# Optimization experiments

Measured on AMD Instinct MI355X. Metric: run time of the kernel, lower is better.

## Reference

```python
import jax, jax.numpy as jnp
import numpy as np

B, L, E, H, DV, V = 256, 512, 200, 256, 30000, 50000
NEG_INF = -jnp.inf

def setup_inputs() -> dict:
    key = jax.random.key(0)
    ks = jax.random.split(key, 16)
    s = 0.05
    f = jnp.float32
    return {
        "input_id": jax.random.randint(ks[0], (B, 1), 0, V),
        "input_emb": jax.random.normal(ks[1], (B, 1, E), f),
        "encoder_outputs": jax.random.normal(ks[2], (B, L, H), f),
        "encoder_input_ids": jax.random.randint(ks[3], (B, L), 0, V),
        "hidden": jax.random.normal(ks[4], (B, 1, H), f),
        "attention": jax.random.normal(ks[5], (B, 1, H), f),
        # GRU (PyTorch layout): W_ih (3H, 2H+E), W_hh (3H, H), gate order r,z,n
        "W_ih": jax.random.normal(ks[6], (3 * H, 2 * H + E), f) * s,
        "W_hh": jax.random.normal(ks[7], (3 * H, H), f) * s,
        "b_ih": jnp.zeros((3 * H,), f),
        "b_hh": jnp.zeros((3 * H,), f),
        "W_attn": jax.random.normal(ks[8], (H, H), f) * s,
        "b_attn": jnp.zeros((H,), f),
        "W_comb": jax.random.normal(ks[9], (H, 2 * H), f) * s,
        "b_comb": jnp.zeros((H,), f),
        "W_gen": jax.random.normal(ks[10], (DV, H), f) * s,
        "b_gen": jnp.zeros((DV,), f),
        "W_copy": jax.random.normal(ks[11], (H, H), f) * s,
        "b_copy": jnp.zeros((H,), f),
    }


def reference(input_id, input_emb, encoder_outputs, encoder_input_ids, hidden,
              attention, W_ih, W_hh, b_ih, b_hh, W_attn, b_attn, W_comb,
              b_comb, W_gen, b_gen, W_copy, b_copy):
    b, l = encoder_input_ids.shape
    # selective read: rou = normalized match mask (NaN guard -> 0)
    mask = (input_id == encoder_input_ids).astype(encoder_outputs.dtype)  # (b,l)
    msum = jnp.sum(mask, axis=1, keepdims=True)
    rou = jnp.where(msum > 0, mask / jnp.where(msum > 0, msum, 1.0), 0.0)
    selective_read = jnp.einsum('bl,blh->bh', rou, encoder_outputs)  # (b,h)

    # GRU single step (dropout is identity at inference)
    x = jnp.concatenate([input_emb[:, 0], attention[:, 0], selective_read], axis=-1)
    h_prev = hidden[:, 0]  # (b,h)
    gx = x @ W_ih.T + b_ih          # (b,3h)
    gh = h_prev @ W_hh.T + b_hh     # (b,3h)
    xr, xz, xn = jnp.split(gx, 3, axis=-1)
    hr, hz, hn = jnp.split(gh, 3, axis=-1)
    r = jax.nn.sigmoid(xr + hr)
    z = jax.nn.sigmoid(xz + hz)
    n = jnp.tanh(xn + r * hn)
    h = (1.0 - z) * n + z * h_prev  # (b,h) cur_hidden

    # attention
    q = h @ W_attn.T + b_attn
    attn_w = jax.nn.softmax(jnp.einsum('bh,blh->bl', q, encoder_outputs), axis=-1)
    attn_applied = jnp.einsum('bl,blh->bh', attn_w, encoder_outputs)
    cur_attention = jnp.tanh(
        jnp.concatenate([attn_applied, h], axis=-1) @ W_comb.T + b_comb)  # (b,h)

    # generate + copy scores, joint softmax
    generate_score = cur_attention @ W_gen.T + b_gen                     # (b,DV)
    copy_weights = jax.nn.sigmoid(encoder_outputs @ W_copy.T + b_copy)   # (b,l,h)
    copy_score = jnp.einsum('blh,bh->bl', copy_weights, cur_attention)   # (b,l)
    score = jax.nn.softmax(jnp.concatenate([generate_score, copy_score], axis=1), axis=1)
    gen_s, copy_s = score[:, :DV], score[:, DV:]

    # fused equivalent of the one-hot scatter/mix: direct scatter-add into vocab
    output = jnp.zeros((b, V), score.dtype)
    output = output.at[:, :DV].add(gen_s)
    output = output.at[jnp.arange(b)[:, None], encoder_input_ids].add(copy_s)

    pos = output > 0
    out = jnp.where(pos, jnp.log(jnp.where(pos, output, 1.0)), NEG_INF)
    return out, h[:, None, :], cur_attention[:, None, :]
```

## Files before the change

kernel.cpp:

```cpp
#include <hip/hip_runtime.h>
#include <cmath>

#define B_  256
#define L_  512
#define E_  200
#define H_  256
#define DV_ 30000
#define V_  50000
#define X_  712
#define G3_ 768

#define NEG_BIG -1.0e30f

typedef __attribute__((ext_vector_type(8))) _Float16 half8;
typedef __attribute__((ext_vector_type(4))) float   floatx4;

#define GLOAD16(gptr, lptr)                                                            \
    __builtin_amdgcn_global_load_lds(                                                  \
        (const __attribute__((address_space(1))) unsigned int*)(gptr),                 \
        (__attribute__((address_space(3))) unsigned int*)(lptr), 16, 0, 0)

__global__ void k_cast_wc(const float* __restrict__ Wc, _Float16* __restrict__ wcb) {
    int i = blockIdx.x * 256 + threadIdx.x;
    wcb[i] = (_Float16)Wc[i];
}

__global__ void k_selread(const int* __restrict__ input_id, const float* __restrict__ emb,
                          const float* __restrict__ attention, const float* __restrict__ hidden,
                          const float* __restrict__ enc, const int* __restrict__ enc_ids,
                          float* __restrict__ xT) {
    int b = blockIdx.x, t = threadIdx.x;
    __shared__ int cnt;
    __shared__ int list[L_];
    if (t == 0) cnt = 0;
    __syncthreads();
    int id = input_id[b];
    for (int l = t; l < L_; l += 256) {
        if (enc_ids[b * L_ + l] == id) { int p = atomicAdd(&cnt, 1); list[p] = l; }
    }
    __syncthreads();
    int n = cnt;
    float s = 0.f;
    for (int i = 0; i < n; i++) s += enc[(b * L_ + list[i]) * H_ + t];
    float sel = (n > 0) ? s / (float)n : 0.f;
    for (int k = t; k < E_; k += 256) xT[k * B_ + b] = emb[b * E_ + k];
    xT[(E_ + t) * B_ + b]       = attention[b * H_ + t];
    xT[(E_ + H_ + t) * B_ + b]  = sel;
    xT[(X_ + t) * B_ + b]       = hidden[b * H_ + t];
}

template<int K>
__global__ void __launch_bounds__(256) k_gru_one(const float* __restrict__ xTp, const float* __restrict__ W,
                                                 const float* __restrict__ bias, float* __restrict__ g) {
    __shared__ __align__(16) float Ws[8 * K];
    int t  = threadIdx.x;
    int j0 = blockIdx.x * 8;
    int bq = t & 63;
    int jh = t >> 6;
#pragma unroll
    for (int jj = 0; jj < 8; jj++) {
        const float4* src = (const float4*)(W + (size_t)(j0 + jj) * K);
        float4* dst = (float4*)(Ws + jj * K);
        for (int i = t; i < K / 4; i += 256) dst[i] = src[i];
    }
    __syncthreads();
    float acc0[4] = {0.f, 0.f, 0.f, 0.f};
    float acc1[4] = {0.f, 0.f, 0.f, 0.f};
    const float* w0 = Ws + (jh * 2 + 0) * K;
    const float* w1 = Ws + (jh * 2 + 1) * K;
#pragma unroll 2
    for (int k4 = 0; k4 < K / 4; k4++) {
        float4 wa = *(const float4*)(w0 + k4 * 4);
        float4 wb = *(const float4*)(w1 + k4 * 4);
        float wav[4] = {wa.x, wa.y, wa.z, wa.w};
        float wbv[4] = {wb.x, wb.y, wb.z, wb.w};
#pragma unroll
        for (int u = 0; u < 4; u++) {
            float4 xv = *(const float4*)(xTp + (size_t)(k4 * 4 + u) * B_ + bq * 4);
            acc0[0] += wav[u] * xv.x; acc0[1] += wav[u] * xv.y;
            acc0[2] += wav[u] * xv.z; acc0[3] += wav[u] * xv.w;
            acc1[0] += wbv[u] * xv.x; acc1[1] += wbv[u] * xv.y;
            acc1[2] += wbv[u] * xv.z; acc1[3] += wbv[u] * xv.w;
        }
    }
    int ja = j0 + jh * 2, jb = ja + 1;
    float ba = bias[ja], bb = bias[jb];
#pragma unroll
    for (int i = 0; i < 4; i++) {
        g[(size_t)(bq * 4 + i) * G3_ + ja] = acc0[i] + ba;
        g[(size_t)(bq * 4 + i) * G3_ + jb] = acc1[i] + bb;
    }
}

__global__ void k_gru_gates(const float* __restrict__ gx, const float* __restrict__ gh,
                            const float* __restrict__ hidden, float* __restrict__ hws,
                            float* __restrict__ hout) {
    int b = blockIdx.x, j = threadIdx.x;
    float xr = gx[b * G3_ + j], xz = gx[b * G3_ + 256 + j], xn = gx[b * G3_ + 512 + j];
    float hr = gh[b * G3_ + j], hz = gh[b * G3_ + 256 + j], hn = gh[b * G3_ + 512 + j];
    float r = 1.f / (1.f + expf(-(xr + hr)));
    float z = 1.f / (1.f + expf(-(xz + hz)));
    float n = tanhf(xn + r * hn);
    float hp = hidden[b * H_ + j];
    float h = (1.f - z) * n + z * hp;
    hws[b * H_ + j] = h;
    hout[b * H_ + j] = h;
}

__global__ void __launch_bounds__(1024) k_attn(const float* __restrict__ hws, const float* __restrict__ enc,
                       const float* __restrict__ W_attn, const float* __restrict__ b_attn,
                       const float* __restrict__ W_comb, const float* __restrict__ b_comb,
                       float* __restrict__ caws, _Float16* __restrict__ cab,
                       float* __restrict__ caout) {
    int b = blockIdx.x, t = threadIdx.x;
    int lane = t & 63, w = t >> 6;
    int jj = t & 255, ph = t >> 8;
    __shared__ float hs[H_], qs[H_], sc[L_], ap[H_];
    __shared__ float part[4][H_];
    __shared__ float red[20];
    if (t < 256) hs[t] = hws[b * H_ + t];
    __syncthreads();
    {
        const float4* wr = (const float4*)(W_attn + (size_t)jj * H_ + ph * 64);
        const float4* hp = (const float4*)(hs + ph * 64);
        float acc = 0.f;
#pragma unroll
        for (int k4 = 0; k4 < 16; k4++) {
            float4 wv = wr[k4]; float4 hv = hp[k4];
            acc += wv.x * hv.x + wv.y * hv.y + wv.z * hv.z + wv.w * hv.w;
        }
        part[ph][jj] = acc;
    }
    __syncthreads();
    if (t < 256) qs[t] = b_attn[t] + part[0][t] + part[1][t] + part[2][t] + part[3][t];
    __syncthreads();
    {
        float4 q4 = *(const float4*)&qs[lane * 4];
        size_t base = (size_t)b * L_ + w * 32;
        for (int i = 0; i < 32; i += 4) {
            float s[4];
#pragma unroll
            for (int u = 0; u < 4; u++) {
                float4 e = *(const float4*)(enc + (base + i + u) * H_ + lane * 4);
                s[u] = q4.x * e.x + q4.y * e.y + q4.z * e.z + q4.w * e.w;
            }
#pragma unroll
            for (int u = 0; u < 4; u++) {
#pragma unroll
                for (int o = 1; o < 64; o <<= 1) s[u] += __shfl_xor(s[u], o);
                if (lane == 0) sc[w * 32 + i + u] = s[u];
            }
        }
    }
    __syncthreads();
    float ev = 0.f;
    if (t < 512) {
        float m = sc[t];
#pragma unroll
        for (int o = 1; o < 64; o <<= 1) m = fmaxf(m, __shfl_xor(m, o));
        if (lane == 0) red[w] = m;
    }
    __syncthreads();
    if (t == 0) {
        float m = red[0];
        for (int i = 1; i < 8; i++) m = fmaxf(m, red[i]);
        red[16] = m;
    }
    __syncthreads();
    if (t < 512) {
        ev = __expf(sc[t] - red[16]);
        float s = ev;
#pragma unroll
        for (int o = 1; o < 64; o <<= 1) s += __shfl_xor(s, o);
        if (lane == 0) red[8 + w] = s;
    }
    __syncthreads();
    if (t == 0) {
        float s = red[8];
        for (int i = 1; i < 8; i++) s += red[8 + i];
        red[17] = 1.f / s;
    }
    __syncthreads();
    if (t < 512) sc[t] = ev * red[17];
    __syncthreads();
    {
        size_t base = (size_t)b * L_ + ph * 128;
        float a0 = 0.f, a1 = 0.f, a2 = 0.f, a3 = 0.f;
        for (int l = 0; l < 128; l += 4) {
            a0 += sc[ph * 128 + l + 0] * enc[(base + l + 0) * H_ + jj];
            a1 += sc[ph * 128 + l + 1] * enc[(base + l + 1) * H_ + jj];
            a2 += sc[ph * 128 + l + 2] * enc[(base + l + 2) * H_ + jj];
            a3 += sc[ph * 128 + l + 3] * enc[(base + l + 3) * H_ + jj];
        }
        part[ph][jj] = (a0 + a1) + (a2 + a3);
    }
    __syncthreads();
    if (t < 256) ap[t] = part[0][t] + part[1][t] + part[2][t] + part[3][t];
    __syncthreads();
    {
        const float4* wr = (const float4*)(W_comb + (size_t)jj * (2 * H_) + ph * 128);
        const float4* xp = (const float4*)(((ph & 2) ? hs : ap) + (ph & 1) * 128);
        float acc = 0.f;
#pragma unroll
        for (int k4 = 0; k4 < 32; k4++) {
            float4 wv = wr[k4]; float4 xv = xp[k4];
            acc += wv.x * xv.x + wv.y * xv.y + wv.z * xv.z + wv.w * xv.w;
        }
        part[ph][jj] = acc;
    }
    __syncthreads();
    if (t < 256) {
        float cav = tanhf(b_comb[t] + part[0][t] + part[1][t] + part[2][t] + part[3][t]);
        caws[b * H_ + t] = cav;
        cab[b * H_ + t]  = (_Float16)cav;
        caout[b * H_ + t] = cav;
    }
}

__global__ void __launch_bounds__(256, 2) k_gen_mfma(
        const _Float16* __restrict__ cab, const float* __restrict__ W_gen,
        const float* __restrict__ b_gen, float* __restrict__ out) {
    __shared__ __align__(16) _Float16 Ah[128 * 32];
    __shared__ __align__(16) float    Bf[128 * 32];
    int t = threadIdx.x, w = t >> 6, lane = t & 63;
    int n0 = blockIdx.x * 128, m0 = blockIdx.y * 128;
    int wm = (w >> 1) * 64, wn = (w & 1) * 64;
    int l15 = lane & 15, q = lane >> 4;
    floatx4 acc[4][4];
#pragma unroll
    for (int i = 0; i < 4; i++)
#pragma unroll
        for (int j = 0; j < 4; j++) acc[i][j] = (floatx4){0.f, 0.f, 0.f, 0.f};

    for (int kc = 0; kc < H_; kc += 32) {
#pragma unroll
        for (int i = 0; i < 2; i++) {
            int t2 = w * 2 + i;
            int row = t2 * 16 + (lane >> 2);
            const _Float16* g = cab + (size_t)(m0 + row) * H_ + kc + (lane & 3) * 8;
            GLOAD16(g, &Ah[t2 * 512]);
        }
#pragma unroll
        for (int i = 0; i < 4; i++) {
            int t2 = w * 4 + i;
            int row = t2 * 8 + (lane >> 3);
            int nn = n0 + row; nn = nn < DV_ ? nn : DV_ - 1;
            const float* g = W_gen + (size_t)nn * H_ + kc + (lane & 7) * 4;
            GLOAD16(g, &Bf[t2 * 256]);
        }
        __syncthreads();
        half8 a[4];
#pragma unroll
        for (int mi = 0; mi < 4; mi++) {
            int m = wm + mi * 16 + l15;
            a[mi] = *(const half8*)&Ah[m * 32 + q * 8];
        }
#pragma unroll
        for (int ni = 0; ni < 4; ni++) {
            int n = wn + ni * 16 + l15;
            const float4* bp = (const float4*)&Bf[n * 32 + q * 8];
            float4 f0 = bp[0], f1 = bp[1];
            half8 bf;
            bf[0] = (_Float16)f0.x; bf[1] = (_Float16)f0.y; bf[2] = (_Float16)f0.z; bf[3] = (_Float16)f0.w;
            bf[4] = (_Float16)f1.x; bf[5] = (_Float16)f1.y; bf[6] = (_Float16)f1.z; bf[7] = (_Float16)f1.w;
#pragma unroll
            for (int mi = 0; mi < 4; mi++)
                acc[mi][ni] = __builtin_amdgcn_mfma_f32_16x16x32_f16(a[mi], bf, acc[mi][ni], 0, 0, 0);
        }
        __syncthreads();
    }
#pragma unroll
    for (int ni = 0; ni < 4; ni++) {
        int col = n0 + wn + ni * 16 + l15;
        if (col < DV_) {
            float bg = b_gen[col];
#pragma unroll
            for (int mi = 0; mi < 4; mi++)
#pragma unroll
                for (int j = 0; j < 4; j++) {
                    int row = m0 + wm + mi * 16 + q * 4 + j;
                    out[(size_t)row * V_ + col] = acc[mi][ni][j] + bg;
                }
        }
    }
}

__global__ void __launch_bounds__(256, 2) k_copy_mfma(
        const float* __restrict__ enc, const _Float16* __restrict__ wcb,
        const float* __restrict__ b_copy, const float* __restrict__ caws,
        float* __restrict__ copy_s) {
    __shared__ __align__(16) float    Af[128 * 32];
    __shared__ __align__(16) _Float16 Bh[256 * 32];
    __shared__ float bcs[H_], cas[H_];
    int t = threadIdx.x, w = t >> 6, lane = t & 63;
    int R0 = blockIdx.x * 128;
    int b  = blockIdx.x >> 2;
    int l15 = lane & 15, q = lane >> 4;
    bcs[t] = b_copy[t];
    cas[t] = caws[b * H_ + t];
    floatx4 acc[2][16];
#pragma unroll
    for (int i = 0; i < 2; i++)
#pragma unroll
        for (int j = 0; j < 16; j++) acc[i][j] = (floatx4){0.f, 0.f, 0.f, 0.f};

    for (int kc = 0; kc < H_; kc += 32) {
#pragma unroll
        for (int i = 0; i < 4; i++) {
            int t2 = w * 4 + i;
            int row = t2 * 8 + (lane >> 3);
            const float* g = enc + (size_t)(R0 + row) * H_ + kc + (lane & 7) * 4;
            GLOAD16(g, &Af[t2 * 256]);
        }
#pragma unroll
        for (int i = 0; i < 4; i++) {
            int t2 = w * 4 + i;
            int row = t2 * 16 + (lane >> 2);
            const _Float16* g = wcb + row * H_ + kc + (lane & 3) * 8;
            GLOAD16(g, &Bh[t2 * 512]);
        }
        __syncthreads();
        half8 a[2];
#pragma unroll
        for (int mi = 0; mi < 2; mi++) {
            int m = w * 32 + mi * 16 + l15;
            const float4* apx = (const float4*)&Af[m * 32 + q * 8];
            float4 f0 = apx[0], f1 = apx[1];
            half8 h;
            h[0] = (_Float16)f0.x; h[1] = (_Float16)f0.y; h[2] = (_Float16)f0.z; h[3] = (_Float16)f0.w;
            h[4] = (_Float16)f1.x; h[5] = (_Float16)f1.y; h[6] = (_Float16)f1.z; h[7] = (_Float16)f1.w;
            a[mi] = h;
        }
#pragma unroll
        for (int ni = 0; ni < 16; ni++) {
            int n = ni * 16 + l15;
            half8 bf = *(const half8*)&Bh[n * 32 + q * 8];
            acc[0][ni] = __builtin_amdgcn_mfma_f32_16x16x32_f16(a[0], bf, acc[0][ni], 0, 0, 0);
            acc[1][ni] = __builtin_amdgcn_mfma_f32_16x16x32_f16(a[1], bf, acc[1][ni], 0, 0, 0);
        }
        __syncthreads();
    }
#pragma unroll
    for (int mi = 0; mi < 2; mi++) {
#pragma unroll
        for (int j = 0; j < 4; j++) {
            float p = 0.f;
#pragma unroll
            for (int ni = 0; ni < 16; ni++) {
                int col = ni * 16 + l15;
                float v = acc[mi][ni][j] + bcs[col];
                p += cas[col] / (1.f + __expf(-v));
            }
            p += __shfl_xor(p, 1);
            p += __shfl_xor(p, 2);
            p += __shfl_xor(p, 4);
            p += __shfl_xor(p, 8);
            if (l15 == 0) copy_s[R0 + w * 32 + mi * 16 + q * 4 + j] = p;
        }
    }
}

__global__ void __launch_bounds__(1024) k_stats(const float* __restrict__ out, const float* __restrict__ copy_s,
                        float* __restrict__ mrow, float* __restrict__ ldrow) {
    int b = blockIdx.x, t = threadIdx.x, lane = t & 63, w = t >> 6;
    __shared__ float rm[16], rs[16];
    const float* row = out + (size_t)b * V_;
    float m = -INFINITY, s = 0.f;
    for (int j = t; j < DV_; j += 1024) {
        float v = row[j];
        if (v > m) { s = s * __expf(m - v) + 1.f; m = v; }
        else       s += __expf(v - m);
    }
    if (t < 512) {
        float v = copy_s[b * L_ + t];
        if (v > m) { s = s * __expf(m - v) + 1.f; m = v; }
        else       s += __expf(v - m);
    }
#pragma unroll
    for (int o = 1; o < 64; o <<= 1) {
        float m2 = __shfl_xor(m, o), s2 = __shfl_xor(s, o);
        float mn = fmaxf(m, m2);
        s = s * __expf(m - mn) + s2 * __expf(m2 - mn);
        m = mn;
    }
    if (lane == 0) { rm[w] = m; rs[w] = s; }
    __syncthreads();
    if (t == 0) {
        float M = rm[0], S = rs[0];
        for (int i = 1; i < 16; i++) {
            float mn = fmaxf(M, rm[i]);
            S = S * __expf(M - mn) + rs[i] * __expf(rm[i] - mn);
            M = mn;
        }
        mrow[b] = M;
        ldrow[b] = __logf(S);
    }
}

__global__ void __launch_bounds__(1024) k_final(float* __restrict__ out, const float* __restrict__ mrow,
                        const float* __restrict__ ldrow) {
    int j = blockIdx.x * 1024 + threadIdx.x;
    int b = blockIdx.y;
    if (j >= V_) return;
    size_t idx = (size_t)b * V_ + j;
    float sh = mrow[b] + ldrow[b];
    out[idx] = (j < DV_) ? out[idx] - sh : NEG_BIG;
}

__global__ void k_scatter_log(float* __restrict__ out, const float* __restrict__ copy_s,
                              const int* __restrict__ enc_ids, const float* __restrict__ mrow,
                              const float* __restrict__ ldrow) {
    int l = blockIdx.x * 256 + threadIdx.x;
    int b = blockIdx.y;
    float p = __expf(copy_s[b * L_ + l] - mrow[b] - ldrow[b]);
    unsigned int* up = (unsigned int*)(out + (size_t)b * V_ + enc_ids[b * L_ + l]);
    unsigned int cur = *up;
    while (true) {
        float ov = __uint_as_float(cur);
        float pv = (ov < -1.0e29f) ? p : __expf(ov) + p;
        unsigned int prev = atomicCAS(up, cur, __float_as_uint(__logf(pv)));
        if (prev == cur) break;
        cur = prev;
    }
}

extern "C" void kernel_launch(void* const* d_in, const int* in_sizes, int n_in,
                              void* d_out, int out_size, void* d_ws, size_t ws_size,
                              hipStream_t stream) {
    const int*   input_id  = (const int*)  d_in[0];
    const float* input_emb = (const float*)d_in[1];
    const float* enc       = (const float*)d_in[2];
    const int*   enc_ids   = (const int*)  d_in[3];
    const float* hidden    = (const float*)d_in[4];
    const float* attention = (const float*)d_in[5];
    const float* W_ih      = (const float*)d_in[6];
    const float* W_hh      = (const float*)d_in[7];
    const float* b_ih      = (const float*)d_in[8];
    const float* b_hh      = (const float*)d_in[9];
    const float* W_attn    = (const float*)d_in[10];
    const float* b_attn    = (const float*)d_in[11];
    const float* W_comb    = (const float*)d_in[12];
    const float* b_comb    = (const float*)d_in[13];
    const float* W_gen     = (const float*)d_in[14];
    const float* b_gen     = (const float*)d_in[15];
    const float* W_copy    = (const float*)d_in[16];
    const float* b_copy    = (const float*)d_in[17];

    float* out = (float*)d_out;
    float* ws  = (float*)d_ws;
    float* xT   = ws;
    float* gx   = xT + 247808;
    float* gh   = gx + 196608;
    float* hws  = gh + 196608;
    float* caws = hws + 65536;
    float* cps  = caws + 65536;
    float* mrow = cps + 131072;
    float* ldrow = mrow + 256;
    _Float16* wcb = (_Float16*)(ldrow + 256);
    _Float16* cab = wcb + 65536;

    float* hout  = out + (size_t)B_ * V_;
    float* caout = hout + B_ * H_;

    k_cast_wc<<<256, 256, 0, stream>>>(W_copy, wcb);
    k_selread<<<256, 256, 0, stream>>>(input_id, input_emb, attention, hidden, enc, enc_ids, xT);
    k_gru_one<712><<<96, 256, 0, stream>>>(xT, W_ih, b_ih, gx);
    k_gru_one<256><<<96, 256, 0, stream>>>(xT + X_ * B_, W_hh, b_hh, gh);
    k_gru_gates<<<256, 256, 0, stream>>>(gx, gh, hidden, hws, hout);
    k_attn<<<256, 1024, 0, stream>>>(hws, enc, W_attn, b_attn, W_comb, b_comb, caws, cab, caout);
    k_gen_mfma<<<dim3((DV_ + 127) / 128, 2), 256, 0, stream>>>(cab, W_gen, b_gen, out);
    k_copy_mfma<<<(B_ * L_) / 128, 256, 0, stream>>>(enc, wcb, b_copy, caws, cps);
    k_stats<<<256, 1024, 0, stream>>>(out, cps, mrow, ldrow);
    dim3 gf((V_ + 1023) / 1024, B_);
    k_final<<<gf, 1024, 0, stream>>>(out, mrow, ldrow);
    dim3 gs(L_ / 256, B_);
    k_scatter_log<<<gs, 256, 0, stream>>>(out, cps, enc_ids, mrow, ldrow);
}
```

Measured before the change: 485.8 us.

## Compute attention scores with split-fp16 MFMA and vectorize attention-applied reduction

The q·enc score computation in k_attn stops using per-row shuffle reductions. Encoder tiles are now staged into LDS with global_load_lds and the dot products run on 16x16x32 fp16 MFMA, with each fp32 operand split into hi/lo halves to keep accuracy close to fp32. The weighted sum over encoder rows now has each wave read float4 rows and writes 16 partial sums, which are then reduced. In exchange the kernel uses a lot more LDS (about 80KB), which can lower occupancy, and it adds extra barriers per k-chunk.

```diff
diff --git a/kernel.cpp b/kernel.cpp
--- a/kernel.cpp
+++ b/kernel.cpp
@@ -115,8 +115,11 @@
     int b = blockIdx.x, t = threadIdx.x;
     int lane = t & 63, w = t >> 6;
     int jj = t & 255, ph = t >> 8;
+    int l15 = lane & 15, q = lane >> 4;
+    __shared__ __align__(16) float Sf[16 * 1024];
     __shared__ float hs[H_], qs[H_], sc[L_], ap[H_];
     __shared__ float part[4][H_];
+    __shared__ float part16[16][H_];
     __shared__ float red[20];
     if (t < 256) hs[t] = hws[b * H_ + t];
     __syncthreads();
@@ -135,20 +138,46 @@
     if (t < 256) qs[t] = b_attn[t] + part[0][t] + part[1][t] + part[2][t] + part[3][t];
     __syncthreads();
     {
-        float4 q4 = *(const float4*)&qs[lane * 4];
-        size_t base = (size_t)b * L_ + w * 32;
-        for (int i = 0; i < 32; i += 4) {
-            float s[4];
-#pragma unroll
-            for (int u = 0; u < 4; u++) {
-                float4 e = *(const float4*)(enc + (base + i + u) * H_ + lane * 4);
-                s[u] = q4.x * e.x + q4.y * e.y + q4.z * e.z + q4.w * e.w;
+        floatx4 acc0 = {0.f, 0.f, 0.f, 0.f}, acc1 = {0.f, 0.f, 0.f, 0.f};
+        float* Sw = Sf + w * 1024;
+        for (int kc = 0; kc < H_; kc += 32) {
+#pragma unroll
+            for (int i = 0; i < 4; i++) {
+                const float* g = enc + ((size_t)b * L_ + w * 32 + i * 8 + (lane >> 3)) * H_
+                                 + kc + (lane & 7) * 4;
+                GLOAD16(g, Sw + i * 256);
             }
-#pragma unroll
-            for (int u = 0; u < 4; u++) {
-#pragma unroll
-                for (int o = 1; o < 64; o <<= 1) s[u] += __shfl_xor(s[u], o);
-                if (lane == 0) sc[w * 32 + i + u] = s[u];
+            __syncthreads();
+            half8 bh, bl;
+#pragma unroll
+            for (int j2 = 0; j2 < 8; j2++) {
+                float v = qs[kc + q * 8 + j2];
+                _Float16 h = (_Float16)v;
+                bh[j2] = h; bl[j2] = (_Float16)(v - (float)h);
+            }
+#pragma unroll
+            for (int tile = 0; tile < 2; tile++) {
+                const float* apx = Sw + (tile * 16 + l15) * 32 + q * 8;
+                half8 ah, al;
+#pragma unroll
+                for (int j2 = 0; j2 < 8; j2++) {
+                    float v = apx[j2];
+                    _Float16 h = (_Float16)v;
+                    ah[j2] = h; al[j2] = (_Float16)(v - (float)h);
+                }
+                floatx4 acc = tile ? acc1 : acc0;
+                acc = __builtin_amdgcn_mfma_f32_16x16x32_f16(al, bh, acc, 0, 0, 0);
+                acc = __builtin_amdgcn_mfma_f32_16x16x32_f16(ah, bl, acc, 0, 0, 0);
+                acc = __builtin_amdgcn_mfma_f32_16x16x32_f16(ah, bh, acc, 0, 0, 0);
+                if (tile) acc1 = acc; else acc0 = acc;
+            }
+            __syncthreads();
+        }
+        if (l15 == 0) {
+#pragma unroll
+            for (int j2 = 0; j2 < 4; j2++) {
+                sc[w * 32 + q * 4 + j2]      = acc0[j2];
+                sc[w * 32 + 16 + q * 4 + j2] = acc1[j2];
             }
         }
     }
@@ -184,18 +213,23 @@
     if (t < 512) sc[t] = ev * red[17];
     __syncthreads();
     {
-        size_t base = (size_t)b * L_ + ph * 128;
-        float a0 = 0.f, a1 = 0.f, a2 = 0.f, a3 = 0.f;
-        for (int l = 0; l < 128; l += 4) {
-            a0 += sc[ph * 128 + l + 0] * enc[(base + l + 0) * H_ + jj];
-            a1 += sc[ph * 128 + l + 1] * enc[(base + l + 1) * H_ + jj];
-            a2 += sc[ph * 128 + l + 2] * enc[(base + l + 2) * H_ + jj];
-            a3 += sc[ph * 128 + l + 3] * enc[(base + l + 3) * H_ + jj];
-        }
-        part[ph][jj] = (a0 + a1) + (a2 + a3);
-    }
-    __syncthreads();
-    if (t < 256) ap[t] = part[0][t] + part[1][t] + part[2][t] + part[3][t];
+        float4 a4 = {0.f, 0.f, 0.f, 0.f};
+        const float4* e4 = (const float4*)enc + ((size_t)b * L_ + w * 32) * 64 + lane;
+#pragma unroll 4
+        for (int r = 0; r < 32; r++) {
+            float s = sc[w * 32 + r];
+            float4 e = e4[(size_t)r * 64];
+            a4.x += s * e.x; a4.y += s * e.y; a4.z += s * e.z; a4.w += s * e.w;
+        }
+        *(float4*)&part16[w][lane * 4] = a4;
+    }
+    __syncthreads();
+    if (t < 256) {
+        float a = 0.f;
+#pragma unroll
+        for (int g = 0; g < 16; g++) a += part16[g][t];
+        ap[t] = a;
+    }
     __syncthreads();
     {
         const float4* wr = (const float4*)(W_comb + (size_t)jj * (2 * H_) + ph * 128);
```

New measurement: 493.5 us. Within noise of the previous version (+1.6%).
